# Performance work log

Measured on AMD Instinct MI355X. Metric: run time of the kernel, lower is better.

Reference implementation:

```python
import jax, jax.numpy as jnp
import numpy as np

D_MODEL = 1024
N_HEADS = 16
HEAD_DIM = D_MODEL // N_HEADS
FF_DIM = 1024  # repo bug: linear2 is Linear(d_model, ff_dim); ff_dim==d_model required for residual
EPS = 1e-5


def _linear_params(k, d_in, d_out):
    kw, kb = jax.random.split(k)
    bound = 1.0 / np.sqrt(d_in)
    W = jax.random.uniform(kw, (d_out, d_in), minval=-bound, maxval=bound, dtype=jnp.float32)
    b = jax.random.uniform(kb, (d_out,), minval=-bound, maxval=bound, dtype=jnp.float32)
    return W, b


def setup_inputs() -> dict:
    key = jax.random.key(0)
    ks = jax.random.split(key, 8)
    src = jax.random.normal(ks[0], (4, 2048, D_MODEL), dtype=jnp.float32)
    Wq, bq = _linear_params(ks[1], D_MODEL, D_MODEL)
    Wk, bk = _linear_params(ks[2], D_MODEL, D_MODEL)
    Wv, bv = _linear_params(ks[3], D_MODEL, D_MODEL)
    Wo, bo = _linear_params(ks[4], D_MODEL, D_MODEL)
    W1, b1 = _linear_params(ks[5], D_MODEL, FF_DIM)
    W2, b2 = _linear_params(ks[6], D_MODEL, FF_DIM)
    g1 = jnp.ones((D_MODEL,), jnp.float32); be1 = jnp.zeros((D_MODEL,), jnp.float32)
    g2 = jnp.ones((D_MODEL,), jnp.float32); be2 = jnp.zeros((D_MODEL,), jnp.float32)
    return {"src": src, "Wq": Wq, "bq": bq, "Wk": Wk, "bk": bk, "Wv": Wv, "bv": bv,
            "Wo": Wo, "bo": bo, "W1": W1, "b1": b1, "W2": W2, "b2": b2,
            "g1": g1, "be1": be1, "g2": g2, "be2": be2}


def _layernorm(x, g, b):
    mu = jnp.mean(x, axis=-1, keepdims=True)
    var = jnp.var(x, axis=-1, keepdims=True)
    return (x - mu) * jax.lax.rsqrt(var + EPS) * g + b


def _mha(x, Wq, bq, Wk, bk, Wv, bv, Wo, bo):
    B, S, _ = x.shape
    def proj(W, b):
        return (x @ W.T + b).reshape(B, S, N_HEADS, HEAD_DIM).transpose(0, 2, 1, 3)
    Q, K, V = proj(Wq, bq), proj(Wk, bk), proj(Wv, bv)
    scale = jnp.float32(np.sqrt(HEAD_DIM))
    energy = jnp.einsum('bhqd,bhkd->bhqk', Q, K) / scale
    attn = jax.nn.softmax(energy, axis=-1)
    out = jnp.einsum('bhqk,bhkd->bhqd', attn, V)
    out = out.transpose(0, 2, 1, 3).reshape(B, S, D_MODEL)
    return out @ Wo.T + bo


def reference(src, Wq, bq, Wk, bk, Wv, bv, Wo, bo, W1, b1, W2, b2, g1, be1, g2, be2):
    x = src
    x = x + _mha(_layernorm(x, g1, be1), Wq, bq, Wk, bk, Wv, bv, Wo, bo)
    h = _layernorm(x, g2, be2)
    ff = jax.nn.relu(h @ W1.T + b1) @ W2.T + b2
    return x + ff
```

## Files before the change

kernel.cpp:

```cpp
#include <hip/hip_runtime.h>
#include <stdint.h>

typedef __attribute__((ext_vector_type(8))) short    bf16x8;
typedef __attribute__((ext_vector_type(4))) short    bf16x4;
typedef __attribute__((ext_vector_type(4))) float    f32x4;
typedef __attribute__((ext_vector_type(8))) uint16_t u16x8;
typedef __attribute__((ext_vector_type(4))) uint16_t u16x4;

#define D_MODEL 1024
#define SEQ     2048
#define NB      4
#define NH      16
#define HD      64
#define MTOK    8192

__device__ __forceinline__ float bf2f(uint16_t u) {
    union { uint32_t i; float f; } x; x.i = ((uint32_t)u) << 16; return x.f;
}
__device__ __forceinline__ uint16_t f2bf(float f) {
    union { float f; uint32_t i; } x; x.f = f;
    uint32_t r = (x.i + 0x7fffu + ((x.i >> 16) & 1u)) >> 16;
    return (uint16_t)r;
}
__device__ __forceinline__ void gload16(const void* g, void* l) {
    __builtin_amdgcn_global_load_lds(
        (const __attribute__((address_space(1))) unsigned int*)g,
        (__attribute__((address_space(3))) unsigned int*)l, 16, 0, 0);
}
__device__ __forceinline__ bf16x8 lds_ld8(const uint16_t* p) {
    bf16x4 a = *(const bf16x4*)p;
    bf16x4 b = *(const bf16x4*)(p + 4);
    bf16x8 r;
    r[0] = a[0]; r[1] = a[1]; r[2] = a[2]; r[3] = a[3];
    r[4] = b[0]; r[5] = b[1]; r[6] = b[2]; r[7] = b[3];
    return r;
}
__device__ __forceinline__ uint32_t pk_bf16_trunc(float lo, float hi) {
    return __builtin_amdgcn_perm(__float_as_uint(hi), __float_as_uint(lo), 0x07060302u);
}

#define VM_WAIT(n) asm volatile("s_waitcnt vmcnt(" #n ")" ::: "memory")
#define RAW_BAR()  __builtin_amdgcn_s_barrier()
#define SCHED_FENCE() __builtin_amdgcn_sched_barrier(0)

__global__ __launch_bounds__(256)
void cvt_all(const float* __restrict__ s0, const float* __restrict__ s1,
             const float* __restrict__ s2, const float* __restrict__ s3,
             const float* __restrict__ s4, const float* __restrict__ s5,
             uint16_t* __restrict__ dQKV, uint16_t* __restrict__ dWo,
             uint16_t* __restrict__ dW1, uint16_t* __restrict__ dW2)
{
    const float* srcs[6] = {s0, s1, s2, s3, s4, s5};
    uint16_t* dsts[6] = {dQKV, dQKV + (size_t)D_MODEL * D_MODEL,
                         dQKV + 2 * (size_t)D_MODEL * D_MODEL, dWo, dW1, dW2};
    const float* in = srcs[blockIdx.y];
    uint16_t* out = dsts[blockIdx.y];
    const int i = (blockIdx.x * 256 + threadIdx.x) * 4;
    float4 v = *(const float4*)(in + i);
    u16x4 o;
    o[0] = f2bf(v.x); o[1] = f2bf(v.y); o[2] = f2bf(v.z); o[3] = f2bf(v.w);
    *(u16x4*)(out + i) = o;
}

__global__ __launch_bounds__(256)
void ln_kernel(const float* __restrict__ x, const float* __restrict__ g,
               const float* __restrict__ be, uint16_t* __restrict__ y)
{
    const int row = blockIdx.x;
    const int tid = threadIdx.x;
    const size_t base = (size_t)row * D_MODEL + tid * 4;
    float4 v = *(const float4*)(x + base);
    float f[4] = {v.x, v.y, v.z, v.w};
    float sum = 0.f, sq = 0.f;
#pragma unroll
    for (int e = 0; e < 4; e++) { sum += f[e]; sq += f[e] * f[e]; }
#pragma unroll
    for (int o = 32; o > 0; o >>= 1) { sum += __shfl_down(sum, o); sq += __shfl_down(sq, o); }
    __shared__ float ps[4], pq[4];
    const int lane = tid & 63, wid = tid >> 6;
    if (lane == 0) { ps[wid] = sum; pq[wid] = sq; }
    __syncthreads();
    const float ts = ps[0] + ps[1] + ps[2] + ps[3];
    const float tq = pq[0] + pq[1] + pq[2] + pq[3];
    const float mean = ts * (1.0f / D_MODEL);
    const float var  = tq * (1.0f / D_MODEL) - mean * mean;
    const float rstd = rsqrtf(var + 1e-5f);
    float4 gv = *(const float4*)(g + tid * 4);
    float4 bv = *(const float4*)(be + tid * 4);
    const float gg[4] = {gv.x, gv.y, gv.z, gv.w};
    const float bb[4] = {bv.x, bv.y, bv.z, bv.w};
    u16x4 outv;
#pragma unroll
    for (int e = 0; e < 4; e++)
        outv[e] = f2bf((f[e] - mean) * rstd * gg[e] + bb[e]);
    *(u16x4*)(y + base) = outv;
}

template<int RESID, int RELU, int OUTF32>
__global__ __launch_bounds__(256, 4)
void gemm_bt64(const uint16_t* __restrict__ A, const uint16_t* __restrict__ W,
               const float* __restrict__ bias, const float* __restrict__ resid,
               void* __restrict__ Cv)
{
    __shared__ uint16_t lA[3][64 * 32];
    __shared__ uint16_t lB[3][128 * 32];
    const int tid  = threadIdx.x;
    const int lane = tid & 63;
    const int quad = lane >> 4;
    const int l16  = lane & 15;
    const int wid  = tid >> 6;
    const int wm   = wid >> 1;
    const int wn   = wid & 1;
    const int m0   = blockIdx.y * 64;
    const int n0   = blockIdx.x * 128;

    f32x4 acc[2][4];
#pragma unroll
    for (int i = 0; i < 2; i++)
#pragma unroll
        for (int j = 0; j < 4; j++) acc[i][j] = (f32x4){0.f, 0.f, 0.f, 0.f};

    const int sr = tid >> 2;
    const int sc = (tid & 3) * 8;
    const uint16_t* gA0 = A + (size_t)(m0 + sr) * D_MODEL + sc;
    const uint16_t* gW0 = W + (size_t)(n0 + sr) * D_MODEL + sc;
    const uint16_t* gW1 = gW0 + (size_t)64 * D_MODEL;

    #define STG_BT(k0, b) do {                        \
        gload16(gA0 + (k0), &lA[b][tid * 8]);         \
        gload16(gW0 + (k0), &lB[b][tid * 8]);         \
        gload16(gW1 + (k0), &lB[b][2048 + tid * 8]);  \
    } while (0)

    #define CMP_BT(b) do {                                                            \
        bf16x8 af[2], bfr[4];                                                         \
        _Pragma("unroll")                                                             \
        for (int i = 0; i < 2; i++)                                                   \
            af[i] = *(const bf16x8*)&lA[b][(wm * 32 + i * 16 + l16) * 32 + quad * 8]; \
        _Pragma("unroll")                                                             \
        for (int j = 0; j < 4; j++)                                                   \
            bfr[j] = *(const bf16x8*)&lB[b][(wn * 64 + j * 16 + l16) * 32 + quad * 8];\
        _Pragma("unroll")                                                             \
        for (int i = 0; i < 2; i++)                                                   \
            _Pragma("unroll")                                                         \
            for (int j = 0; j < 4; j++)                                               \
                acc[i][j] = __builtin_amdgcn_mfma_f32_16x16x32_bf16(af[i], bfr[j], acc[i][j], 0, 0, 0); \
    } while (0)

    STG_BT(0, 0); STG_BT(32, 1); STG_BT(64, 2);
    for (int i = 0; i < 29; ++i) {
        VM_WAIT(6);
        RAW_BAR();
        SCHED_FENCE();
        const int p = i % 3;
        CMP_BT(p);
        SCHED_FENCE();
        RAW_BAR();
        STG_BT((i + 3) * 32, p);
    }
    VM_WAIT(6); RAW_BAR(); SCHED_FENCE(); CMP_BT(2); SCHED_FENCE();
    VM_WAIT(3); RAW_BAR(); SCHED_FENCE(); CMP_BT(0); SCHED_FENCE();
    VM_WAIT(0); RAW_BAR(); SCHED_FENCE(); CMP_BT(1);
    #undef STG_BT
    #undef CMP_BT

#pragma unroll
    for (int j = 0; j < 4; j++) {
        const int col = n0 + wn * 64 + j * 16 + l16;
        const float bvv = bias[col];
#pragma unroll
        for (int i = 0; i < 2; i++) {
            const int row = m0 + wm * 32 + i * 16 + quad * 4;
#pragma unroll
            for (int r = 0; r < 4; r++) {
                float v = acc[i][j][r] + bvv;
                const size_t idx = (size_t)(row + r) * D_MODEL + col;
                if (RESID) v += resid[idx];
                if (RELU)  v = fmaxf(v, 0.0f);
                if (OUTF32) ((float*)Cv)[idx] = v;
                else        ((uint16_t*)Cv)[idx] = f2bf(v);
            }
        }
    }
}

#define QSCALE 0.18033688f
__global__ __launch_bounds__(256, 3)
void gemm_qkv(const uint16_t* __restrict__ A, const uint16_t* __restrict__ Wqkv,
              const float* __restrict__ bq, const float* __restrict__ bk,
              const float* __restrict__ bv, uint16_t* __restrict__ Qb,
              uint16_t* __restrict__ Kb, uint16_t* __restrict__ Vt)
{
    __shared__ uint16_t lA[3][128 * 32];
    __shared__ uint16_t lB[3][128 * 32];
    const int tid  = threadIdx.x;
    const int lane = tid & 63;
    const int quad = lane >> 4;
    const int l16  = lane & 15;
    const int wid  = tid >> 6;
    const int wm   = wid >> 1;
    const int wn   = wid & 1;
    const int t0   = blockIdx.y * 128;
    const int n0   = blockIdx.x * 128;
    const int which = n0 >> 10;
    const int lc0   = n0 & 1023;

    f32x4 acc[4][4];
#pragma unroll
    for (int i = 0; i < 4; i++)
#pragma unroll
        for (int j = 0; j < 4; j++) acc[i][j] = (f32x4){0.f, 0.f, 0.f, 0.f};

    const int sr = tid >> 2;
    const int sc = (tid & 3) * 8;
    const uint16_t* gA0 = A + (size_t)(t0 + sr) * D_MODEL + sc;
    const uint16_t* gA1 = gA0 + (size_t)64 * D_MODEL;
    const uint16_t* gW0 = Wqkv + (size_t)(n0 + sr) * D_MODEL + sc;
    const uint16_t* gW1 = gW0 + (size_t)64 * D_MODEL;

    #define STG_QKV(k0, b) do {                       \
        gload16(gA0 + (k0), &lA[b][tid * 8]);         \
        gload16(gA1 + (k0), &lA[b][2048 + tid * 8]);  \
        gload16(gW0 + (k0), &lB[b][tid * 8]);         \
        gload16(gW1 + (k0), &lB[b][2048 + tid * 8]);  \
    } while (0)

    #define CMP_QKV(b) do {                                                               \
        bf16x8 fa[4], fb[4];                                                              \
        if (which != 2) {                                                                 \
            _Pragma("unroll")                                                             \
            for (int i = 0; i < 4; i++)                                                   \
                fa[i] = *(const bf16x8*)&lA[b][(wm * 64 + i * 16 + l16) * 32 + quad * 8]; \
            _Pragma("unroll")                                                             \
            for (int j = 0; j < 4; j++)                                                   \
                fb[j] = *(const bf16x8*)&lB[b][(wn * 64 + j * 16 + l16) * 32 + quad * 8]; \
        } else {                                                                          \
            _Pragma("unroll")                                                             \
            for (int i = 0; i < 4; i++)                                                   \
                fa[i] = *(const bf16x8*)&lB[b][(wm * 64 + i * 16 + l16) * 32 + quad * 8]; \
            _Pragma("unroll")                                                             \
            for (int j = 0; j < 4; j++)                                                   \
                fb[j] = *(const bf16x8*)&lA[b][(wn * 64 + j * 16 + l16) * 32 + quad * 8]; \
        }                                                                                 \
        _Pragma("unroll")                                                                 \
        for (int i = 0; i < 4; i++)                                                       \
            _Pragma("unroll")                                                             \
            for (int j = 0; j < 4; j++)                                                   \
                acc[i][j] = __builtin_amdgcn_mfma_f32_16x16x32_bf16(fa[i], fb[j], acc[i][j], 0, 0, 0); \
    } while (0)

    STG_QKV(0, 0); STG_QKV(32, 1); STG_QKV(64, 2);
    for (int i = 0; i < 29; ++i) {
        VM_WAIT(8);
        RAW_BAR();
        SCHED_FENCE();
        const int p = i % 3;
        CMP_QKV(p);
        SCHED_FENCE();
        RAW_BAR();
        STG_QKV((i + 3) * 32, p);
    }
    VM_WAIT(8); RAW_BAR(); SCHED_FENCE(); CMP_QKV(2); SCHED_FENCE();
    VM_WAIT(4); RAW_BAR(); SCHED_FENCE(); CMP_QKV(0); SCHED_FENCE();
    VM_WAIT(0); RAW_BAR(); SCHED_FENCE(); CMP_QKV(1);
    #undef STG_QKV
    #undef CMP_QKV

    if (which != 2) {
        const float* bias = (which == 0) ? bq : bk;
        uint16_t* C = (which == 0) ? Qb : Kb;
        const float alpha = (which == 0) ? QSCALE : 1.0f;
#pragma unroll
        for (int j = 0; j < 4; j++) {
            const int col = lc0 + wn * 64 + j * 16 + l16;
            const float bvv = bias[col];
#pragma unroll
            for (int i = 0; i < 4; i++) {
                const int row = t0 + wm * 64 + i * 16 + quad * 4;
#pragma unroll
                for (int r = 0; r < 4; r++)
                    C[(size_t)(row + r) * D_MODEL + col] = f2bf((acc[i][j][r] + bvv) * alpha);
            }
        }
    } else {
#pragma unroll
        for (int i = 0; i < 4; i++) {
#pragma unroll
            for (int r = 0; r < 4; r++) {
                const int wrow = lc0 + wm * 64 + i * 16 + quad * 4 + r;
                const float bvv = bv[wrow];
#pragma unroll
                for (int j = 0; j < 4; j++) {
                    const int tok = t0 + wn * 64 + j * 16 + l16;
                    Vt[(size_t)wrow * MTOK + tok] = f2bf(acc[i][j][r] + bvv);
                }
            }
        }
    }
}

#define PST 68
__global__ __launch_bounds__(256, 4)
void attn_kernel(const uint16_t* __restrict__ Q, const uint16_t* __restrict__ K,
                 const uint16_t* __restrict__ Vt, uint16_t* __restrict__ O)
{
    __shared__ uint16_t sQP[128 * PST];
    __shared__ uint16_t sK [64 * PST];
    __shared__ uint16_t sVt[64 * PST];
    __shared__ float    sSt[128];

    const int tid  = threadIdx.x;
    const int lane = tid & 63;
    const int quad = lane >> 4;
    const int l16  = lane & 15;
    const int w    = tid >> 6;

    const int bh = blockIdx.x;
    const int h  = bh & (NH - 1);
    const int b  = bh >> 4;
    const int q0 = blockIdx.y * 128;
    const size_t headoff = (size_t)h * HD;
    const size_t bbase   = (size_t)b * SEQ;

    const int r8 = tid >> 3;
    const int c8 = (tid & 7) * 8;

#pragma unroll
    for (int i = 0; i < 4; i++)
        gload16(Q + (bbase + q0 + i * 32 + r8) * D_MODEL + headoff + c8, &sQP[i * 2048 + tid * 8]);
    __syncthreads();

    bf16x8 qa[2][2];
#pragma unroll
    for (int i = 0; i < 2; i++)
#pragma unroll
        for (int ks = 0; ks < 2; ks++)
            qa[i][ks] = *(const bf16x8*)&sQP[(w * 32 + i * 16 + l16) * 64 + ks * 32 + quad * 8];

    f32x4 oacc[2][4];
#pragma unroll
    for (int i = 0; i < 2; i++)
#pragma unroll
        for (int n = 0; n < 4; n++) oacc[i][n] = (f32x4){0.f, 0.f, 0.f, 0.f};
    float lrun[2] = {0.f, 0.f};

    const uint16_t* gK  = K  + bbase * D_MODEL + headoff;
    const uint16_t* gVt = Vt + headoff * MTOK + bbase;

    for (int kv0 = 0; kv0 < SEQ; kv0 += 64) {
        u16x8 kreg[2], vreg[2];
#pragma unroll
        for (int i = 0; i < 2; i++) {
            const int row = i * 32 + r8;
            kreg[i] = *(const u16x8*)(gK + (size_t)(kv0 + row) * D_MODEL + c8);
            vreg[i] = *(const u16x8*)(gVt + (size_t)row * MTOK + kv0 + c8);
        }
        __syncthreads();
#pragma unroll
        for (int i = 0; i < 2; i++) {
            const int row = i * 32 + r8;
            *(u16x4*)&sK [(size_t)row * PST + c8]     = (u16x4){kreg[i][0], kreg[i][1], kreg[i][2], kreg[i][3]};
            *(u16x4*)&sK [(size_t)row * PST + c8 + 4] = (u16x4){kreg[i][4], kreg[i][5], kreg[i][6], kreg[i][7]};
            *(u16x4*)&sVt[(size_t)row * PST + c8]     = (u16x4){vreg[i][0], vreg[i][1], vreg[i][2], vreg[i][3]};
            *(u16x4*)&sVt[(size_t)row * PST + c8 + 4] = (u16x4){vreg[i][4], vreg[i][5], vreg[i][6], vreg[i][7]};
        }
        __syncthreads();

        f32x4 st[4][2];
#pragma unroll
        for (int j = 0; j < 4; j++)
#pragma unroll
            for (int i = 0; i < 2; i++) st[j][i] = (f32x4){0.f, 0.f, 0.f, 0.f};
#pragma unroll
        for (int ks = 0; ks < 2; ks++)
#pragma unroll
            for (int j = 0; j < 4; j++) {
                bf16x8 kb = lds_ld8(&sK[(j * 16 + l16) * PST + ks * 32 + quad * 8]);
#pragma unroll
                for (int i = 0; i < 2; i++)
                    st[j][i] = __builtin_amdgcn_mfma_f32_16x16x32_bf16(kb, qa[i][ks], st[j][i], 0, 0, 0);
            }

#pragma unroll
        for (int i = 0; i < 2; i++) {
            float rs = 0.f;
#pragma unroll
            for (int j = 0; j < 4; j++) {
#pragma unroll
                for (int r = 0; r < 4; r++) {
                    const float p = __builtin_amdgcn_exp2f(st[j][i][r]);
                    st[j][i][r] = p;
                    rs += p;
                }
            }
            lrun[i] += rs;
#pragma unroll
            for (int j = 0; j < 4; j++) {
                uint2 pk;
                pk.x = pk_bf16_trunc(st[j][i][0], st[j][i][1]);
                pk.y = pk_bf16_trunc(st[j][i][2], st[j][i][3]);
                *(uint2*)&sQP[(size_t)(w * 32 + i * 16 + l16) * PST + j * 16 + quad * 4] = pk;
            }
        }

#pragma unroll
        for (int i = 0; i < 2; i++)
#pragma unroll
            for (int ks = 0; ks < 2; ks++) {
                bf16x8 pa = lds_ld8(&sQP[(size_t)(w * 32 + i * 16 + l16) * PST + ks * 32 + quad * 8]);
#pragma unroll
                for (int n = 0; n < 4; n++) {
                    bf16x8 vb = lds_ld8(&sVt[(n * 16 + l16) * PST + ks * 32 + quad * 8]);
                    oacc[i][n] = __builtin_amdgcn_mfma_f32_16x16x32_bf16(pa, vb, oacc[i][n], 0, 0, 0);
                }
            }
    }

#pragma unroll
    for (int i = 0; i < 2; i++) {
        lrun[i] += __shfl_xor(lrun[i], 16);
        lrun[i] += __shfl_xor(lrun[i], 32);
        sSt[w * 32 + i * 16 + l16] = 1.0f / lrun[i];
    }
#pragma unroll
    for (int i = 0; i < 2; i++)
#pragma unroll
        for (int r = 0; r < 4; r++) {
            const size_t row = bbase + q0 + w * 32 + i * 16 + quad * 4 + r;
            const float inv = sSt[w * 32 + i * 16 + quad * 4 + r];
#pragma unroll
            for (int n = 0; n < 4; n++)
                O[row * D_MODEL + headoff + n * 16 + l16] = f2bf(oacc[i][n][r] * inv);
        }
}

extern "C" void kernel_launch(void* const* d_in, const int* in_sizes, int n_in,
                              void* d_out, int out_size, void* d_ws, size_t ws_size,
                              hipStream_t stream)
{
    const float* src = (const float*)d_in[0];
    const float* Wq  = (const float*)d_in[1];
    const float* bq  = (const float*)d_in[2];
    const float* Wk  = (const float*)d_in[3];
    const float* bk  = (const float*)d_in[4];
    const float* Wv  = (const float*)d_in[5];
    const float* bv  = (const float*)d_in[6];
    const float* Wo  = (const float*)d_in[7];
    const float* bo  = (const float*)d_in[8];
    const float* W1  = (const float*)d_in[9];
    const float* b1  = (const float*)d_in[10];
    const float* W2  = (const float*)d_in[11];
    const float* b2  = (const float*)d_in[12];
    const float* g1  = (const float*)d_in[13];
    const float* be1 = (const float*)d_in[14];
    const float* g2  = (const float*)d_in[15];
    const float* be2 = (const float*)d_in[16];
    float* out = (float*)d_out;

    uint16_t* ws  = (uint16_t*)d_ws;
    const size_t BUF = (size_t)MTOK * D_MODEL;
    const size_t WSZ = (size_t)D_MODEL * D_MODEL;
    uint16_t* xn1  = ws;
    uint16_t* Vtb  = ws + BUF;
    uint16_t* wQKV = ws + 2 * BUF;
    uint16_t* wWo  = wQKV + 3 * WSZ;
    uint16_t* wW1  = wWo + WSZ;
    uint16_t* wW2  = wW1 + WSZ;
    uint16_t* Qb   = (uint16_t*)d_out;
    uint16_t* Kb   = Qb + BUF;
    float*    x2   = (float*)d_out;

    dim3 blk(256);
    cvt_all<<<dim3(1024, 6), 256, 0, stream>>>(Wq, Wk, Wv, Wo, W1, W2, wQKV, wWo, wW1, wW2);
    ln_kernel<<<8192, 256, 0, stream>>>(src, g1, be1, xn1);
    gemm_qkv<<<dim3(24, 64), blk, 0, stream>>>(xn1, wQKV, bq, bk, bv, Qb, Kb, Vtb);
    attn_kernel<<<dim3(64, 16), 256, 0, stream>>>(Qb, Kb, Vtb, xn1);
    gemm_bt64<1, 0, 1><<<dim3(8, 128), blk, 0, stream>>>(xn1, wWo, bo, src, x2);
    ln_kernel<<<8192, 256, 0, stream>>>(x2, g2, be2, xn1);
    gemm_bt64<0, 1, 0><<<dim3(8, 128), blk, 0, stream>>>(xn1, wW1, b1, nullptr, Vtb);
    gemm_bt64<1, 0, 1><<<dim3(8, 128), blk, 0, stream>>>(Vtb, wW2, b2, x2, out);
}
```

Before: 381.0 us.

## Enlarge GEMM block tiles to 256x128 with 512-thread workgroups

Both the QKV projection GEMM and the generic bias/residual GEMM now use 512-thread blocks, each covering 256 rows by 128 columns with 8 waves arranged 4x2 (or 2x4 for the transposed V path). Grid sizes and global-load staging change to match, and the vmcnt wait counts drop because each thread now issues three loads per stage. The goal is more reuse of each staged A and W tile per block and fewer total blocks, cutting global and L2 traffic. In exchange, per-block LDS use and register pressure rise, occupancy falls to two blocks per CU, and the grids have fewer blocks to spread across the CUs.

```diff
diff --git a/kernel.cpp b/kernel.cpp
--- a/kernel.cpp
+++ b/kernel.cpp
@@ -97,12 +97,12 @@
 }
 
 template<int RESID, int RELU, int OUTF32>
-__global__ __launch_bounds__(256, 4)
-void gemm_bt64(const uint16_t* __restrict__ A, const uint16_t* __restrict__ W,
-               const float* __restrict__ bias, const float* __restrict__ resid,
-               void* __restrict__ Cv)
-{
-    __shared__ uint16_t lA[3][64 * 32];
+__global__ __launch_bounds__(512, 2)
+void gemm_bt(const uint16_t* __restrict__ A, const uint16_t* __restrict__ W,
+             const float* __restrict__ bias, const float* __restrict__ resid,
+             void* __restrict__ Cv)
+{
+    __shared__ uint16_t lA[3][256 * 32];
     __shared__ uint16_t lB[3][128 * 32];
     const int tid  = threadIdx.x;
     const int lane = tid & 63;
@@ -111,40 +111,40 @@
     const int wid  = tid >> 6;
     const int wm   = wid >> 1;
     const int wn   = wid & 1;
-    const int m0   = blockIdx.y * 64;
+    const int m0   = blockIdx.y * 256;
     const int n0   = blockIdx.x * 128;
 
-    f32x4 acc[2][4];
-#pragma unroll
-    for (int i = 0; i < 2; i++)
+    f32x4 acc[4][4];
+#pragma unroll
+    for (int i = 0; i < 4; i++)
 #pragma unroll
         for (int j = 0; j < 4; j++) acc[i][j] = (f32x4){0.f, 0.f, 0.f, 0.f};
 
     const int sr = tid >> 2;
     const int sc = (tid & 3) * 8;
     const uint16_t* gA0 = A + (size_t)(m0 + sr) * D_MODEL + sc;
+    const uint16_t* gA1 = gA0 + (size_t)128 * D_MODEL;
     const uint16_t* gW0 = W + (size_t)(n0 + sr) * D_MODEL + sc;
-    const uint16_t* gW1 = gW0 + (size_t)64 * D_MODEL;
 
     #define STG_BT(k0, b) do {                        \
         gload16(gA0 + (k0), &lA[b][tid * 8]);         \
+        gload16(gA1 + (k0), &lA[b][4096 + tid * 8]);  \
         gload16(gW0 + (k0), &lB[b][tid * 8]);         \
-        gload16(gW1 + (k0), &lB[b][2048 + tid * 8]);  \
     } while (0)
 
     #define CMP_BT(b) do {                                                            \
-        bf16x8 af[2], bfr[4];                                                         \
+        bf16x8 fa[4], fb[4];                                                          \
         _Pragma("unroll")                                                             \
-        for (int i = 0; i < 2; i++)                                                   \
-            af[i] = *(const bf16x8*)&lA[b][(wm * 32 + i * 16 + l16) * 32 + quad * 8]; \
+        for (int i = 0; i < 4; i++)                                                   \
+            fa[i] = *(const bf16x8*)&lA[b][(wm * 64 + i * 16 + l16) * 32 + quad * 8]; \
         _Pragma("unroll")                                                             \
         for (int j = 0; j < 4; j++)                                                   \
-            bfr[j] = *(const bf16x8*)&lB[b][(wn * 64 + j * 16 + l16) * 32 + quad * 8];\
+            fb[j] = *(const bf16x8*)&lB[b][(wn * 64 + j * 16 + l16) * 32 + quad * 8]; \
         _Pragma("unroll")                                                             \
-        for (int i = 0; i < 2; i++)                                                   \
+        for (int i = 0; i < 4; i++)                                                   \
             _Pragma("unroll")                                                         \
             for (int j = 0; j < 4; j++)                                               \
-                acc[i][j] = __builtin_amdgcn_mfma_f32_16x16x32_bf16(af[i], bfr[j], acc[i][j], 0, 0, 0); \
+                acc[i][j] = __builtin_amdgcn_mfma_f32_16x16x32_bf16(fa[i], fb[j], acc[i][j], 0, 0, 0); \
     } while (0)
 
     STG_BT(0, 0); STG_BT(32, 1); STG_BT(64, 2);
@@ -169,8 +169,8 @@
         const int col = n0 + wn * 64 + j * 16 + l16;
         const float bvv = bias[col];
 #pragma unroll
-        for (int i = 0; i < 2; i++) {
-            const int row = m0 + wm * 32 + i * 16 + quad * 4;
+        for (int i = 0; i < 4; i++) {
+            const int row = m0 + wm * 64 + i * 16 + quad * 4;
 #pragma unroll
             for (int r = 0; r < 4; r++) {
                 float v = acc[i][j][r] + bvv;
@@ -185,13 +185,13 @@
 }
 
 #define QSCALE 0.18033688f
-__global__ __launch_bounds__(256, 3)
+__global__ __launch_bounds__(512, 2)
 void gemm_qkv(const uint16_t* __restrict__ A, const uint16_t* __restrict__ Wqkv,
               const float* __restrict__ bq, const float* __restrict__ bk,
               const float* __restrict__ bv, uint16_t* __restrict__ Qb,
               uint16_t* __restrict__ Kb, uint16_t* __restrict__ Vt)
 {
-    __shared__ uint16_t lA[3][128 * 32];
+    __shared__ uint16_t lA[3][256 * 32];
     __shared__ uint16_t lB[3][128 * 32];
     const int tid  = threadIdx.x;
     const int lane = tid & 63;
@@ -200,7 +200,9 @@
     const int wid  = tid >> 6;
     const int wm   = wid >> 1;
     const int wn   = wid & 1;
-    const int t0   = blockIdx.y * 128;
+    const int wmv  = wid >> 2;
+    const int wnv  = wid & 3;
+    const int t0   = blockIdx.y * 256;
     const int n0   = blockIdx.x * 128;
     const int which = n0 >> 10;
     const int lc0   = n0 & 1023;
@@ -214,15 +216,13 @@
     const int sr = tid >> 2;
     const int sc = (tid & 3) * 8;
     const uint16_t* gA0 = A + (size_t)(t0 + sr) * D_MODEL + sc;
-    const uint16_t* gA1 = gA0 + (size_t)64 * D_MODEL;
+    const uint16_t* gA1 = gA0 + (size_t)128 * D_MODEL;
     const uint16_t* gW0 = Wqkv + (size_t)(n0 + sr) * D_MODEL + sc;
-    const uint16_t* gW1 = gW0 + (size_t)64 * D_MODEL;
 
     #define STG_QKV(k0, b) do {                       \
         gload16(gA0 + (k0), &lA[b][tid * 8]);         \
-        gload16(gA1 + (k0), &lA[b][2048 + tid * 8]);  \
+        gload16(gA1 + (k0), &lA[b][4096 + tid * 8]);  \
         gload16(gW0 + (k0), &lB[b][tid * 8]);         \
-        gload16(gW1 + (k0), &lB[b][2048 + tid * 8]);  \
     } while (0)
 
     #define CMP_QKV(b) do {                                                               \
@@ -237,10 +237,10 @@
         } else {                                                                          \
             _Pragma("unroll")                                                             \
             for (int i = 0; i < 4; i++)                                                   \
-                fa[i] = *(const bf16x8*)&lB[b][(wm * 64 + i * 16 + l16) * 32 + quad * 8]; \
+                fa[i] = *(const bf16x8*)&lB[b][(wmv * 64 + i * 16 + l16) * 32 + quad * 8];\
             _Pragma("unroll")                                                             \
             for (int j = 0; j < 4; j++)                                                   \
-                fb[j] = *(const bf16x8*)&lA[b][(wn * 64 + j * 16 + l16) * 32 + quad * 8]; \
+                fb[j] = *(const bf16x8*)&lA[b][(wnv * 64 + j * 16 + l16) * 32 + quad * 8];\
         }                                                                                 \
         _Pragma("unroll")                                                                 \
         for (int i = 0; i < 4; i++)                                                       \
@@ -251,7 +251,7 @@
 
     STG_QKV(0, 0); STG_QKV(32, 1); STG_QKV(64, 2);
     for (int i = 0; i < 29; ++i) {
-        VM_WAIT(8);
+        VM_WAIT(6);
         RAW_BAR();
         SCHED_FENCE();
         const int p = i % 3;
@@ -260,8 +260,8 @@
         RAW_BAR();
         STG_QKV((i + 3) * 32, p);
     }
-    VM_WAIT(8); RAW_BAR(); SCHED_FENCE(); CMP_QKV(2); SCHED_FENCE();
-    VM_WAIT(4); RAW_BAR(); SCHED_FENCE(); CMP_QKV(0); SCHED_FENCE();
+    VM_WAIT(6); RAW_BAR(); SCHED_FENCE(); CMP_QKV(2); SCHED_FENCE();
+    VM_WAIT(3); RAW_BAR(); SCHED_FENCE(); CMP_QKV(0); SCHED_FENCE();
     VM_WAIT(0); RAW_BAR(); SCHED_FENCE(); CMP_QKV(1);
     #undef STG_QKV
     #undef CMP_QKV
@@ -287,11 +287,11 @@
         for (int i = 0; i < 4; i++) {
 #pragma unroll
             for (int r = 0; r < 4; r++) {
-                const int wrow = lc0 + wm * 64 + i * 16 + quad * 4 + r;
+                const int wrow = lc0 + wmv * 64 + i * 16 + quad * 4 + r;
                 const float bvv = bv[wrow];
 #pragma unroll
                 for (int j = 0; j < 4; j++) {
-                    const int tok = t0 + wn * 64 + j * 16 + l16;
+                    const int tok = t0 + wnv * 64 + j * 16 + l16;
                     Vt[(size_t)wrow * MTOK + tok] = f2bf(acc[i][j][r] + bvv);
                 }
             }
@@ -470,13 +470,13 @@
     uint16_t* Kb   = Qb + BUF;
     float*    x2   = (float*)d_out;
 
-    dim3 blk(256);
+    dim3 blk512(512);
     cvt_all<<<dim3(1024, 6), 256, 0, stream>>>(Wq, Wk, Wv, Wo, W1, W2, wQKV, wWo, wW1, wW2);
     ln_kernel<<<8192, 256, 0, stream>>>(src, g1, be1, xn1);
-    gemm_qkv<<<dim3(24, 64), blk, 0, stream>>>(xn1, wQKV, bq, bk, bv, Qb, Kb, Vtb);
+    gemm_qkv<<<dim3(24, 32), blk512, 0, stream>>>(xn1, wQKV, bq, bk, bv, Qb, Kb, Vtb);
     attn_kernel<<<dim3(64, 16), 256, 0, stream>>>(Qb, Kb, Vtb, xn1);
-    gemm_bt64<1, 0, 1><<<dim3(8, 128), blk, 0, stream>>>(xn1, wWo, bo, src, x2);
+    gemm_bt<1, 0, 1><<<dim3(8, 32), blk512, 0, stream>>>(xn1, wWo, bo, src, x2);
     ln_kernel<<<8192, 256, 0, stream>>>(x2, g2, be2, xn1);
-    gemm_bt64<0, 1, 0><<<dim3(8, 128), blk, 0, stream>>>(xn1, wW1, b1, nullptr, Vtb);
-    gemm_bt64<1, 0, 1><<<dim3(8, 128), blk, 0, stream>>>(Vtb, wW2, b2, x2, out);
-}
+    gemm_bt<0, 1, 0><<<dim3(8, 32), blk512, 0, stream>>>(xn1, wW1, b1, nullptr, Vtb);
+    gemm_bt<1, 0, 1><<<dim3(8, 32), blk512, 0, stream>>>(Vtb, wW2, b2, x2, out);
+}
```

New measurement: 427.5 us. 12.2% more time.

## Load weight fragments directly from global into registers, dropping LDS staging

Applied to the files above, without the earlier changes.

Both GEMM kernels stop staging the weight tile through shared memory. Each wave now loads its own B fragments straight from global memory into registers right before the MFMAs, so only the activation tile goes through LDS and the triple buffering. This halves the LDS footprint, which is why the QKV kernel's occupancy hint is raised from 3 to 4. The cost is that the weight loads are issued synchronously each k-step with no prefetch depth, so global latency may be exposed, and weight rows shared between waves are fetched redundantly.

```diff
diff --git a/kernel.cpp b/kernel.cpp
--- a/kernel.cpp
+++ b/kernel.cpp
@@ -103,7 +103,6 @@
                void* __restrict__ Cv)
 {
     __shared__ uint16_t lA[3][64 * 32];
-    __shared__ uint16_t lB[3][128 * 32];
     const int tid  = threadIdx.x;
     const int lane = tid & 63;
     const int quad = lane >> 4;
@@ -123,33 +122,31 @@
     const int sr = tid >> 2;
     const int sc = (tid & 3) * 8;
     const uint16_t* gA0 = A + (size_t)(m0 + sr) * D_MODEL + sc;
-    const uint16_t* gW0 = W + (size_t)(n0 + sr) * D_MODEL + sc;
-    const uint16_t* gW1 = gW0 + (size_t)64 * D_MODEL;
-
-    #define STG_BT(k0, b) do {                        \
-        gload16(gA0 + (k0), &lA[b][tid * 8]);         \
-        gload16(gW0 + (k0), &lB[b][tid * 8]);         \
-        gload16(gW1 + (k0), &lB[b][2048 + tid * 8]);  \
+    const uint16_t* gB = W + (size_t)(n0 + wn * 64 + l16) * D_MODEL + quad * 8;
+
+    bf16x8 wf[4];
+    #define STG_BT(k0, b)  gload16(gA0 + (k0), &lA[b][tid * 8])
+    #define LDB_BT(k0) do {                                                   \
+        _Pragma("unroll")                                                     \
+        for (int j = 0; j < 4; j++)                                           \
+            wf[j] = *(const bf16x8*)(gB + (size_t)(j * 16) * D_MODEL + (k0)); \
     } while (0)
-
     #define CMP_BT(b) do {                                                            \
-        bf16x8 af[2], bfr[4];                                                         \
+        bf16x8 af[2];                                                                 \
         _Pragma("unroll")                                                             \
         for (int i = 0; i < 2; i++)                                                   \
             af[i] = *(const bf16x8*)&lA[b][(wm * 32 + i * 16 + l16) * 32 + quad * 8]; \
         _Pragma("unroll")                                                             \
-        for (int j = 0; j < 4; j++)                                                   \
-            bfr[j] = *(const bf16x8*)&lB[b][(wn * 64 + j * 16 + l16) * 32 + quad * 8];\
-        _Pragma("unroll")                                                             \
         for (int i = 0; i < 2; i++)                                                   \
             _Pragma("unroll")                                                         \
             for (int j = 0; j < 4; j++)                                               \
-                acc[i][j] = __builtin_amdgcn_mfma_f32_16x16x32_bf16(af[i], bfr[j], acc[i][j], 0, 0, 0); \
+                acc[i][j] = __builtin_amdgcn_mfma_f32_16x16x32_bf16(af[i], wf[j], acc[i][j], 0, 0, 0); \
     } while (0)
 
     STG_BT(0, 0); STG_BT(32, 1); STG_BT(64, 2);
     for (int i = 0; i < 29; ++i) {
-        VM_WAIT(6);
+        VM_WAIT(2);
+        LDB_BT(i * 32);
         RAW_BAR();
         SCHED_FENCE();
         const int p = i % 3;
@@ -158,10 +155,11 @@
         RAW_BAR();
         STG_BT((i + 3) * 32, p);
     }
-    VM_WAIT(6); RAW_BAR(); SCHED_FENCE(); CMP_BT(2); SCHED_FENCE();
-    VM_WAIT(3); RAW_BAR(); SCHED_FENCE(); CMP_BT(0); SCHED_FENCE();
-    VM_WAIT(0); RAW_BAR(); SCHED_FENCE(); CMP_BT(1);
+    VM_WAIT(2); LDB_BT(29 * 32); RAW_BAR(); SCHED_FENCE(); CMP_BT(2); SCHED_FENCE();
+    VM_WAIT(1); LDB_BT(30 * 32); RAW_BAR(); SCHED_FENCE(); CMP_BT(0); SCHED_FENCE();
+    VM_WAIT(0); LDB_BT(31 * 32); RAW_BAR(); SCHED_FENCE(); CMP_BT(1);
     #undef STG_BT
+    #undef LDB_BT
     #undef CMP_BT
 
 #pragma unroll
@@ -185,14 +183,13 @@
 }
 
 #define QSCALE 0.18033688f
-__global__ __launch_bounds__(256, 3)
+__global__ __launch_bounds__(256, 4)
 void gemm_qkv(const uint16_t* __restrict__ A, const uint16_t* __restrict__ Wqkv,
               const float* __restrict__ bq, const float* __restrict__ bk,
               const float* __restrict__ bv, uint16_t* __restrict__ Qb,
               uint16_t* __restrict__ Kb, uint16_t* __restrict__ Vt)
 {
     __shared__ uint16_t lA[3][128 * 32];
-    __shared__ uint16_t lB[3][128 * 32];
     const int tid  = threadIdx.x;
     const int lane = tid & 63;
     const int quad = lane >> 4;
@@ -215,43 +212,47 @@
     const int sc = (tid & 3) * 8;
     const uint16_t* gA0 = A + (size_t)(t0 + sr) * D_MODEL + sc;
     const uint16_t* gA1 = gA0 + (size_t)64 * D_MODEL;
-    const uint16_t* gW0 = Wqkv + (size_t)(n0 + sr) * D_MODEL + sc;
-    const uint16_t* gW1 = gW0 + (size_t)64 * D_MODEL;
-
+    const int wrbase = (which != 2) ? wn * 64 : wm * 64;
+    const uint16_t* gB = Wqkv + (size_t)(n0 + wrbase + l16) * D_MODEL + quad * 8;
+
+    bf16x8 wf[4];
     #define STG_QKV(k0, b) do {                       \
         gload16(gA0 + (k0), &lA[b][tid * 8]);         \
         gload16(gA1 + (k0), &lA[b][2048 + tid * 8]);  \
-        gload16(gW0 + (k0), &lB[b][tid * 8]);         \
-        gload16(gW1 + (k0), &lB[b][2048 + tid * 8]);  \
     } while (0)
-
+    #define LDB_QKV(k0) do {                                                  \
+        _Pragma("unroll")                                                     \
+        for (int t = 0; t < 4; t++)                                           \
+            wf[t] = *(const bf16x8*)(gB + (size_t)(t * 16) * D_MODEL + (k0)); \
+    } while (0)
     #define CMP_QKV(b) do {                                                               \
-        bf16x8 fa[4], fb[4];                                                              \
         if (which != 2) {                                                                 \
+            bf16x8 fa[4];                                                                 \
             _Pragma("unroll")                                                             \
             for (int i = 0; i < 4; i++)                                                   \
                 fa[i] = *(const bf16x8*)&lA[b][(wm * 64 + i * 16 + l16) * 32 + quad * 8]; \
             _Pragma("unroll")                                                             \
-            for (int j = 0; j < 4; j++)                                                   \
-                fb[j] = *(const bf16x8*)&lB[b][(wn * 64 + j * 16 + l16) * 32 + quad * 8]; \
+            for (int i = 0; i < 4; i++)                                                   \
+                _Pragma("unroll")                                                         \
+                for (int j = 0; j < 4; j++)                                               \
+                    acc[i][j] = __builtin_amdgcn_mfma_f32_16x16x32_bf16(fa[i], wf[j], acc[i][j], 0, 0, 0); \
         } else {                                                                          \
-            _Pragma("unroll")                                                             \
-            for (int i = 0; i < 4; i++)                                                   \
-                fa[i] = *(const bf16x8*)&lB[b][(wm * 64 + i * 16 + l16) * 32 + quad * 8]; \
+            bf16x8 fb[4];                                                                 \
             _Pragma("unroll")                                                             \
             for (int j = 0; j < 4; j++)                                                   \
                 fb[j] = *(const bf16x8*)&lA[b][(wn * 64 + j * 16 + l16) * 32 + quad * 8]; \
+            _Pragma("unroll")                                                             \
+            for (int i = 0; i < 4; i++)                                                   \
+                _Pragma("unroll")                                                         \
+                for (int j = 0; j < 4; j++)                                               \
+                    acc[i][j] = __builtin_amdgcn_mfma_f32_16x16x32_bf16(wf[i], fb[j], acc[i][j], 0, 0, 0); \
         }                                                                                 \
-        _Pragma("unroll")                                                                 \
-        for (int i = 0; i < 4; i++)                                                       \
-            _Pragma("unroll")                                                             \
-            for (int j = 0; j < 4; j++)                                                   \
-                acc[i][j] = __builtin_amdgcn_mfma_f32_16x16x32_bf16(fa[i], fb[j], acc[i][j], 0, 0, 0); \
     } while (0)
 
     STG_QKV(0, 0); STG_QKV(32, 1); STG_QKV(64, 2);
     for (int i = 0; i < 29; ++i) {
-        VM_WAIT(8);
+        VM_WAIT(4);
+        LDB_QKV(i * 32);
         RAW_BAR();
         SCHED_FENCE();
         const int p = i % 3;
@@ -260,10 +261,11 @@
         RAW_BAR();
         STG_QKV((i + 3) * 32, p);
     }
-    VM_WAIT(8); RAW_BAR(); SCHED_FENCE(); CMP_QKV(2); SCHED_FENCE();
-    VM_WAIT(4); RAW_BAR(); SCHED_FENCE(); CMP_QKV(0); SCHED_FENCE();
-    VM_WAIT(0); RAW_BAR(); SCHED_FENCE(); CMP_QKV(1);
+    VM_WAIT(4); LDB_QKV(29 * 32); RAW_BAR(); SCHED_FENCE(); CMP_QKV(2); SCHED_FENCE();
+    VM_WAIT(2); LDB_QKV(30 * 32); RAW_BAR(); SCHED_FENCE(); CMP_QKV(0); SCHED_FENCE();
+    VM_WAIT(0); LDB_QKV(31 * 32); RAW_BAR(); SCHED_FENCE(); CMP_QKV(1);
     #undef STG_QKV
+    #undef LDB_QKV
     #undef CMP_QKV
 
     if (which != 2) {
```

New measurement: 801.9 us. 110% more time.
